# Performance work log

Hardware: AMD Instinct MI355X
Metric: run time of the kernel (lower is better)

Reference implementation:

```python
import jax, jax.numpy as jnp
import numpy as np

N_NODES = 10000
N_EDGES = 100000
IN_CH = 384
PROJ = 768  # in_channels * projection_factor
N_BLOCKS = 4
OUT_CH = 128
LN_EPS = 1e-5


def _p(key, shape, fan_in):
    return jax.random.normal(key, shape, dtype=jnp.float32) * (1.0 / np.sqrt(fan_in))


def setup_inputs() -> dict:
    key = jax.random.key(0)
    ks = iter(jax.random.split(key, 64))
    x = jax.random.normal(next(ks), (N_NODES, IN_CH), dtype=jnp.float32)
    edge_index = jax.random.randint(next(ks), (2, N_EDGES), 0, N_NODES, dtype=jnp.int64)
    inp = {
        'x': x,
        'edge_index': edge_index,
        'proj_W': _p(next(ks), (PROJ, IN_CH), IN_CH),
        'proj_b': jnp.zeros((PROJ,), jnp.float32),
        'norm_w': jnp.ones((N_BLOCKS, PROJ), jnp.float32),
        'norm_b': jnp.zeros((N_BLOCKS, PROJ), jnp.float32),
        'g1_W': _p(next(ks), (N_BLOCKS, 4 * 192, PROJ), PROJ),
        'g1_as': _p(next(ks), (N_BLOCKS, 4, 192), 192),
        'g1_ad': _p(next(ks), (N_BLOCKS, 4, 192), 192),
        'g1_b': jnp.zeros((N_BLOCKS, 4 * 192), jnp.float32),
        'g2_W': _p(next(ks), (N_BLOCKS, 2 * 96, PROJ), PROJ),
        'g2_as': _p(next(ks), (N_BLOCKS, 2, 96), 96),
        'g2_ad': _p(next(ks), (N_BLOCKS, 2, 96), 96),
        'g2_b': jnp.zeros((N_BLOCKS, 2 * 96), jnp.float32),
        'uni_W': _p(next(ks), (N_BLOCKS, PROJ, 960), 960),
        'uni_b': jnp.zeros((N_BLOCKS, PROJ), jnp.float32),
        'fnorm_w': jnp.ones((PROJ,), jnp.float32),
        'fnorm_b': jnp.zeros((PROJ,), jnp.float32),
        'fg_W': _p(next(ks), (8 * OUT_CH, PROJ), PROJ),
        'fg_as': _p(next(ks), (8, OUT_CH), OUT_CH),
        'fg_ad': _p(next(ks), (8, OUT_CH), OUT_CH),
        'fg_b': jnp.zeros((OUT_CH,), jnp.float32),
    }
    return inp


def layer_norm(x, w, b):
    m = x.mean(-1, keepdims=True)
    v = ((x - m) ** 2).mean(-1, keepdims=True)
    return (x - m) / jnp.sqrt(v + LN_EPS) * w + b


def gat_conv(x, src, dst, W, a_src, a_dst, bias, heads, out_ch, concat):
    # PyG GATConv (eval mode, add_self_loops already applied in src/dst).
    n = x.shape[0]
    h = (x @ W.T).reshape(n, heads, out_ch)          # [N,H,C]
    al_s = jnp.einsum('nhc,hc->nh', h, a_src)        # [N,H]
    al_d = jnp.einsum('nhc,hc->nh', h, a_dst)
    e = jax.nn.leaky_relu(al_s[src] + al_d[dst], 0.2)  # [E,H]
    emax = jax.ops.segment_max(e, dst, num_segments=n)
    ee = jnp.exp(e - emax[dst])
    den = jax.ops.segment_sum(ee, dst, num_segments=n)
    alpha = ee / (den[dst] + 1e-16)                  # softmax over incoming edges
    out = jax.ops.segment_sum(h[src] * alpha[:, :, None], dst, num_segments=n)
    out = out.reshape(n, heads * out_ch) if concat else out.mean(axis=1)
    return out + bias


def reference(x, edge_index, proj_W, proj_b, norm_w, norm_b,
              g1_W, g1_as, g1_ad, g1_b, g2_W, g2_as, g2_ad, g2_b,
              uni_W, uni_b, fnorm_w, fnorm_b, fg_W, fg_as, fg_ad, fg_b):
    n = x.shape[0]
    loop = jnp.arange(n, dtype=edge_index.dtype)
    src = jnp.concatenate([edge_index[0], loop])  # add self loops (PyG default)
    dst = jnp.concatenate([edge_index[1], loop])

    h = jax.nn.elu(x @ proj_W.T + proj_b)
    for i in range(N_BLOCKS):
        res = h
        hn = layer_norm(h, norm_w[i], norm_b[i])
        o1 = gat_conv(hn, src, dst, g1_W[i], g1_as[i], g1_ad[i], g1_b[i], 4, 192, True)
        o2 = gat_conv(hn, src, dst, g2_W[i], g2_as[i], g2_ad[i], g2_b[i], 2, 96, True)
        cat = jax.nn.elu(jnp.concatenate([o1, o2], axis=-1))  # [N,960]
        h = jax.nn.elu(res + cat @ uni_W[i].T + uni_b[i])
    h = layer_norm(h, fnorm_w, fnorm_b)
    return gat_conv(h, src, dst, fg_W, fg_as, fg_ad, fg_b, 8, OUT_CH, False)
```

## Files before the change

kernel.cpp:

```cpp
#include <hip/hip_runtime.h>
#include <math.h>

#define N_NODES 10000
#define N_EDGES 100000
#define E_TOT   (N_EDGES + N_NODES)
#define PROJ    768
#define LN_EPS  1e-5f

typedef __attribute__((ext_vector_type(8))) short bf16x8;
typedef __attribute__((ext_vector_type(4))) short bf16x4;
typedef __attribute__((ext_vector_type(4))) float f32x4;

__device__ __forceinline__ float elu_f(float x){ return x > 0.f ? x : __expf(x) - 1.f; }
__device__ __forceinline__ float bf2f(unsigned short u){ return __uint_as_float(((unsigned int)u) << 16); }
__device__ __forceinline__ unsigned short f2bf(float f){
  unsigned int u = __float_as_uint(f);
  return (unsigned short)((u + 0x7FFFu + ((u >> 16) & 1u)) >> 16);
}

#define GLOAD16(gp, lp) __builtin_amdgcn_global_load_lds((const __attribute__((address_space(1))) void*)(gp), (__attribute__((address_space(3))) void*)(lp), 16, 0, 0)

__global__ void k_count(const int* __restrict__ ei, int* __restrict__ cnt){
  int e = blockIdx.x*blockDim.x + threadIdx.x;
  if (e >= E_TOT) return;
  int dst = (e < N_EDGES) ? ei[N_EDGES + e] : (e - N_EDGES);
  atomicAdd(&cnt[dst], 1);
}

__global__ void k_scan(const int* __restrict__ cnt, int* __restrict__ indptr){
  __shared__ int s[1024];
  __shared__ int s_running;
  int t = threadIdx.x;
  if (t == 0) s_running = 0;
  __syncthreads();
  for (int base = 0; base < N_NODES; base += 1024){
    int v = (base + t < N_NODES) ? cnt[base + t] : 0;
    s[t] = v; __syncthreads();
    for (int off = 1; off < 1024; off <<= 1){
      int add = (t >= off) ? s[t - off] : 0;
      __syncthreads();
      s[t] += add;
      __syncthreads();
    }
    int total = s[1023];
    int run = s_running;
    if (base + t < N_NODES) indptr[base + t] = run + s[t] - v;
    __syncthreads();
    if (t == 0) s_running = run + total;
    __syncthreads();
  }
  if (t == 0) indptr[N_NODES] = s_running;
}

__global__ void k_copy_int(const int* __restrict__ src, int* __restrict__ dst, int n){
  int i = blockIdx.x*blockDim.x + threadIdx.x;
  if (i < n) dst[i] = src[i];
}

__global__ void k_fill(const int* __restrict__ ei, int* __restrict__ pos, int* __restrict__ csr_src){
  int e = blockIdx.x*blockDim.x + threadIdx.x;
  if (e >= E_TOT) return;
  int s, d;
  if (e < N_EDGES){ s = ei[e]; d = ei[N_EDGES + e]; }
  else            { s = d = e - N_EDGES; }
  int p = atomicAdd(&pos[d], 1);
  csr_src[p] = s;
}

__global__ void k_f2bf_arr4(const float4* __restrict__ in, ushort4* __restrict__ out, int n4){
  int i = blockIdx.x*blockDim.x + threadIdx.x;
  if (i < n4){
    float4 v = in[i];
    ushort4 o;
    o.x = f2bf(v.x); o.y = f2bf(v.y); o.z = f2bf(v.z); o.w = f2bf(v.w);
    out[i] = o;
  }
}

__global__ void k_pack_l1l2(const float* __restrict__ g1, const float* __restrict__ g2,
                            unsigned short* __restrict__ dst){
  int i = blockIdx.x*blockDim.x + threadIdx.x;
  if (i >= 737280) return;
  int layer = i / 184320;
  int off4  = i - layer*184320;
  float4 v;
  if (off4 < 147456) v = *((const float4*)(g1 + (size_t)layer*589824) + off4);
  else               v = *((const float4*)(g2 + (size_t)layer*147456) + (off4 - 147456));
  ushort4 o;
  o.x = f2bf(v.x); o.y = f2bf(v.y); o.z = f2bf(v.z); o.w = f2bf(v.w);
  ((ushort4*)(dst + (size_t)layer*737280))[off4] = o;
}

__global__ void k_layernorm_bf(const float* __restrict__ x, const float* __restrict__ w,
                               const float* __restrict__ b, unsigned short* __restrict__ y){
  int n = blockIdx.x;
  int t = threadIdx.x;
  const float* xr = x + (size_t)n*PROJ;
  float v0 = xr[t], v1 = xr[t+256], v2 = xr[t+512];
  float s  = v0+v1+v2;
  float s2 = v0*v0 + v1*v1 + v2*v2;
  #pragma unroll
  for (int off = 32; off; off >>= 1){ s += __shfl_down(s, off); s2 += __shfl_down(s2, off); }
  __shared__ float rs[4], rs2[4];
  __shared__ float s_mean, s_rstd;
  int wid = t >> 6, lane = t & 63;
  if (lane == 0){ rs[wid] = s; rs2[wid] = s2; }
  __syncthreads();
  if (t == 0){
    float S  = rs[0]+rs[1]+rs[2]+rs[3];
    float S2 = rs2[0]+rs2[1]+rs2[2]+rs2[3];
    float m  = S * (1.f/768.f);
    float var = S2 * (1.f/768.f) - m*m;
    s_mean = m; s_rstd = rsqrtf(var + LN_EPS);
  }
  __syncthreads();
  float m = s_mean, r = s_rstd;
  unsigned short* yr = y + (size_t)n*PROJ;
  yr[t]     = f2bf((v0-m)*r*w[t]     + b[t]);
  yr[t+256] = f2bf((v1-m)*r*w[t+256] + b[t+256]);
  yr[t+512] = f2bf((v2-m)*r*w[t+512] + b[t+512]);
}

template<int EPI>
__global__ __launch_bounds__(256, 2)
void k_gemm_mfma(const unsigned short* __restrict__ A, int lda,
                 const unsigned short* __restrict__ W,
                 void* __restrict__ Cv, int ldc,
                 int M, int N, int K,
                 const float* __restrict__ bias,
                 const float* __restrict__ res, int ldres, int NBN){
  __shared__ unsigned short As[2][128*64];
  __shared__ unsigned short Bs[2][128*64];
  const int tid = threadIdx.x;
  const int lane = tid & 63, wid = tid >> 6;
  const int wm = wid >> 1, wn = wid & 1;

  const int nwg = gridDim.x;
  const int q = nwg >> 3, r = nwg & 7;
  const int xcd = blockIdx.x & 7, o = blockIdx.x >> 3;
  const int swz = (xcd < r ? xcd*(q+1) : r*(q+1) + (xcd - r)*q) + o;
  const int bm = (swz / NBN) * 128;
  const int bn = (swz % NBN) * 128;

  const int srow = tid >> 3;
  const int sc16 = (tid & 7) ^ (srow & 7);
  size_t ga[4], gb[4];
  #pragma unroll
  for (int p = 0; p < 4; p++){
    ga[p] = (size_t)min(bm + p*32 + srow, M-1)*lda + sc16*8;
    gb[p] = (size_t)min(bn + p*32 + srow, N-1)*K   + sc16*8;
  }
  const int ldst = tid*8;

  f32x4 acc[4][4];
  #pragma unroll
  for (int i=0;i<4;i++)
    #pragma unroll
    for (int j=0;j<4;j++) acc[i][j] = (f32x4){0.f,0.f,0.f,0.f};

  const int rA = wm*64 + (lane & 15);
  const int rB = wn*64 + (lane & 15);

  const int NT = K >> 6;
  int cur = 0;
  #pragma unroll
  for (int p = 0; p < 4; p++){
    GLOAD16(A + ga[p], &As[0][p*2048 + ldst]);
    GLOAD16(W + gb[p], &Bs[0][p*2048 + ldst]);
  }
  for (int t = 0; t < NT; ++t){
    __syncthreads();
    if (t + 1 < NT){
      const int k0 = (t+1) << 6;
      #pragma unroll
      for (int p = 0; p < 4; p++){
        GLOAD16(A + ga[p] + k0, &As[cur^1][p*2048 + ldst]);
        GLOAD16(W + gb[p] + k0, &Bs[cur^1][p*2048 + ldst]);
      }
    }
    #pragma unroll
    for (int kk = 0; kk < 2; kk++){
      bf16x8 af[4], bfr[4];
      const int cA = (((kk<<2) | (lane>>4)) ^ (lane&7)) * 8;
      #pragma unroll
      for (int mi = 0; mi < 4; mi++)
        af[mi] = *(const bf16x8*)&As[cur][(rA + mi*16)*64 + cA];
      #pragma unroll
      for (int ni = 0; ni < 4; ni++)
        bfr[ni] = *(const bf16x8*)&Bs[cur][(rB + ni*16)*64 + cA];
      #pragma unroll
      for (int mi = 0; mi < 4; mi++)
        #pragma unroll
        for (int ni = 0; ni < 4; ni++)
          acc[mi][ni] = __builtin_amdgcn_mfma_f32_16x16x32_bf16(af[mi], bfr[ni], acc[mi][ni], 0,0,0);
    }
    cur ^= 1;
  }

  const int mrow0 = bm + wm*64 + ((lane>>4)<<2);
  const int ncol0 = bn + wn*64 + (lane & 15);
  #pragma unroll
  for (int mi=0; mi<4; mi++){
    #pragma unroll
    for (int rr=0; rr<4; rr++){
      int m = mrow0 + mi*16 + rr;
      if (m >= M) continue;
      #pragma unroll
      for (int ni=0; ni<4; ni++){
        int n = ncol0 + ni*16;
        if (n >= N) continue;
        float v = acc[mi][ni][rr];
        if (EPI == 0){
          ((unsigned short*)Cv)[(size_t)m*ldc + n] = f2bf(v);
        } else if (EPI == 1){
          ((float*)Cv)[(size_t)m*ldc + n] = elu_f(v + bias[n]);
        } else {
          ((float*)Cv)[(size_t)m*ldc + n] = elu_f(v + bias[n] + res[(size_t)m*ldres + n]);
        }
      }
    }
  }
}

template<int H, int C>
__global__ void k_attn_coef(const unsigned short* __restrict__ hlin, int ldh,
                            const float* __restrict__ a_src,
                            const float* __restrict__ a_dst,
                            float* __restrict__ als, float* __restrict__ ald){
  constexpr int CH = C/4;
  int n = blockIdx.x;
  int wid = threadIdx.x >> 6, lane = threadIdx.x & 63;
  float ss = 0.f, sd = 0.f;
  if (lane < CH){
    bf16x4 hv = *(const bf16x4*)(hlin + (size_t)n*ldh + wid*C + lane*4);
    float4 as_ = *(const float4*)&a_src[wid*C + lane*4];
    float4 ad_ = *(const float4*)&a_dst[wid*C + lane*4];
    float h0 = bf2f((unsigned short)hv.x), h1 = bf2f((unsigned short)hv.y);
    float h2 = bf2f((unsigned short)hv.z), h3 = bf2f((unsigned short)hv.w);
    ss = h0*as_.x + h1*as_.y + h2*as_.z + h3*as_.w;
    sd = h0*ad_.x + h1*ad_.y + h2*ad_.z + h3*ad_.w;
  }
  #pragma unroll
  for (int off = 32; off; off >>= 1){ ss += __shfl_down(ss, off); sd += __shfl_down(sd, off); }
  if (lane == 0){ als[n*H + wid] = ss; ald[n*H + wid] = sd; }
}

template<int H, int C, bool CONCAT, bool DO_ELU>
__global__ __launch_bounds__(256)
void k_attn_agg(const unsigned short* __restrict__ hlin, int ldh,
                const float* __restrict__ als, const float* __restrict__ ald,
                const int* __restrict__ indptr, const int* __restrict__ csr_src,
                const float* __restrict__ bias,
                void* __restrict__ outv, int ldo, int col0){
  constexpr int TOT = H*C;
  constexpr int CHUNKS = TOT/4;
  constexpr int CPL = (CHUNKS + 63)/64;
  int n = blockIdx.x;
  int tid = threadIdx.x;
  int wv = tid >> 6, lane = tid & 63;
  int beg = indptr[n], end = indptr[n+1];

  __shared__ float s_m[H], s_dinv[H], s_ald[H];
  __shared__ float s_red[4][TOT];

  for (int h = wv; h < H; h += 4){
    float aldv = ald[n*H + h];
    float m = -1e30f, d = 0.f;
    for (int e = beg + lane; e < end; e += 64){
      int s = csr_src[e];
      float v = als[s*H + h] + aldv;
      v = v > 0.f ? v : 0.2f*v;
      if (v > m){ d *= __expf(m - v); m = v; }
      d += __expf(v - m);
    }
    #pragma unroll
    for (int off = 1; off < 64; off <<= 1){
      float mo = __shfl_xor(m, off);
      float dd = __shfl_xor(d, off);
      float mn = fmaxf(m, mo);
      d = d*__expf(m - mn) + dd*__expf(mo - mn);
      m = mn;
    }
    if (lane == 0){ s_m[h] = m; s_dinv[h] = 1.f/(d + 1e-16f); s_ald[h] = aldv; }
  }
  __syncthreads();

  int hof[CPL];
  #pragma unroll
  for (int p = 0; p < CPL; p++) hof[p] = ((lane + p*64)*4)/C;

  f32x4 acc[CPL];
  #pragma unroll
  for (int p = 0; p < CPL; p++) acc[p] = (f32x4){0.f,0.f,0.f,0.f};

  for (int e = beg + wv; e < end; e += 4){
    int s = csr_src[e];
    float al = 0.f;
    if (lane < H){
      float v = als[s*H + lane] + s_ald[lane];
      v = v > 0.f ? v : 0.2f*v;
      al = __expf(v - s_m[lane]) * s_dinv[lane];
    }
    float aph[CPL];
    #pragma unroll
    for (int p = 0; p < CPL; p++) aph[p] = __shfl(al, hof[p]);
    const bf16x4* hr = (const bf16x4*)(hlin + (size_t)s*ldh);
    #pragma unroll
    for (int p = 0; p < CPL; p++){
      int ch = lane + p*64;
      if (CHUNKS % 64 == 0 || ch < CHUNKS){
        bf16x4 hv = hr[ch];
        acc[p].x += bf2f((unsigned short)hv.x)*aph[p];
        acc[p].y += bf2f((unsigned short)hv.y)*aph[p];
        acc[p].z += bf2f((unsigned short)hv.z)*aph[p];
        acc[p].w += bf2f((unsigned short)hv.w)*aph[p];
      }
    }
  }

  #pragma unroll
  for (int p = 0; p < CPL; p++){
    int ch = lane + p*64;
    if (CHUNKS % 64 == 0 || ch < CHUNKS)
      *(f32x4*)&s_red[wv][ch*4] = acc[p];
  }
  __syncthreads();

  if (CONCAT){
    unsigned short* out = (unsigned short*)outv;
    constexpr int QS = (TOT + 255)/256;
    #pragma unroll
    for (int qq = 0; qq < QS; qq++){
      int idx = tid + qq*256;
      if (TOT % 256 == 0 || idx < TOT){
        float v = s_red[0][idx] + s_red[1][idx] + s_red[2][idx] + s_red[3][idx] + bias[idx];
        if (DO_ELU) v = elu_f(v);
        out[(size_t)n*ldo + col0 + idx] = f2bf(v);
      }
    }
  } else {
    float* out = (float*)outv;
    if (tid < C){
      float v = 0.f;
      #pragma unroll
      for (int h = 0; h < H; h++){
        int idx = h*C + tid;
        v += s_red[0][idx] + s_red[1][idx] + s_red[2][idx] + s_red[3][idx];
      }
      out[(size_t)n*ldo + tid] = v*(1.f/(float)H) + bias[tid];
    }
  }
}

extern "C" void kernel_launch(void* const* d_in, const int* in_sizes, int n_in,
                              void* d_out, int out_size, void* d_ws, size_t ws_size,
                              hipStream_t stream){
  const float* x      = (const float*)d_in[0];
  const int*   ei     = (const int*)  d_in[1];
  const float* proj_W = (const float*)d_in[2];
  const float* proj_b = (const float*)d_in[3];
  const float* norm_w = (const float*)d_in[4];
  const float* norm_b = (const float*)d_in[5];
  const float* g1_W   = (const float*)d_in[6];
  const float* g1_as  = (const float*)d_in[7];
  const float* g1_ad  = (const float*)d_in[8];
  const float* g1_b   = (const float*)d_in[9];
  const float* g2_W   = (const float*)d_in[10];
  const float* g2_as  = (const float*)d_in[11];
  const float* g2_ad  = (const float*)d_in[12];
  const float* g2_b   = (const float*)d_in[13];
  const float* uni_W  = (const float*)d_in[14];
  const float* uni_b  = (const float*)d_in[15];
  const float* fnorm_w= (const float*)d_in[16];
  const float* fnorm_b= (const float*)d_in[17];
  const float* fg_W   = (const float*)d_in[18];
  const float* fg_as  = (const float*)d_in[19];
  const float* fg_ad  = (const float*)d_in[20];
  const float* fg_b   = (const float*)d_in[21];

  float* w = (float*)d_ws;
  float* h    = w; w += 7680000;
  float* h2   = w; w += 7680000;
  unsigned short* linbuf = (unsigned short*)w; w += 5120000;
  unsigned short* hnb  = (unsigned short*)w; w += 3840000;
  unsigned short* catb = (unsigned short*)w; w += 4800000;
  unsigned short* wb   = (unsigned short*)w; w += 3489792;
  float* als  = w; w += 80000;
  float* ald  = w; w += 80000;
  float* als2 = w; w += 80000;
  float* ald2 = w; w += 80000;
  int* iw = (int*)w;
  int* cnt     = iw; iw += 10016;
  int* indptr  = iw; iw += 10016;
  int* pos     = iw; iw += 10016;
  int* csr_src = iw; iw += 110016;

  unsigned short* wb_proj = wb;
  unsigned short* wb_l12  = wb_proj + 294912;
  unsigned short* wb_uni  = wb_l12 + 2949120;
  unsigned short* wb_fg   = wb_uni + 2949120;

  hipMemsetAsync(cnt, 0, N_NODES*sizeof(int), stream);
  k_count<<<(E_TOT+255)/256, 256, 0, stream>>>(ei, cnt);
  k_scan<<<1, 1024, 0, stream>>>(cnt, indptr);
  k_copy_int<<<(N_NODES+255)/256, 256, 0, stream>>>(indptr, pos, N_NODES);
  k_fill<<<(E_TOT+255)/256, 256, 0, stream>>>(ei, pos, csr_src);

  k_f2bf_arr4<<<(960000+255)/256, 256, 0, stream>>>((const float4*)x, (ushort4*)hnb, 960000);
  k_f2bf_arr4<<<(73728+255)/256,  256, 0, stream>>>((const float4*)proj_W, (ushort4*)wb_proj, 73728);
  k_pack_l1l2<<<(737280+255)/256, 256, 0, stream>>>(g1_W, g2_W, wb_l12);
  k_f2bf_arr4<<<(737280+255)/256, 256, 0, stream>>>((const float4*)uni_W, (ushort4*)wb_uni, 737280);
  k_f2bf_arr4<<<(196608+255)/256, 256, 0, stream>>>((const float4*)fg_W, (ushort4*)wb_fg, 196608);

  dim3 blk(256);
  const int GM = (N_NODES + 127) / 128;

  k_gemm_mfma<1><<<dim3(6*GM), blk, 0, stream>>>(hnb, 384, wb_proj, h, 768, N_NODES, 768, 384, proj_b, nullptr, 0, 6);

  float* cur = h;
  float* oth = h2;
  for (int i = 0; i < 4; i++){
    k_layernorm_bf<<<N_NODES, 256, 0, stream>>>(cur, norm_w + i*768, norm_b + i*768, hnb);
    k_gemm_mfma<0><<<dim3(8*GM), blk, 0, stream>>>(hnb, 768, wb_l12 + (size_t)i*737280, linbuf, 960, N_NODES, 960, 768, nullptr, nullptr, 0, 8);
    k_attn_coef<4,192><<<N_NODES, 256, 0, stream>>>(linbuf, 960, g1_as + i*768, g1_ad + i*768, als, ald);
    k_attn_agg<4,192,true,true><<<N_NODES, 256, 0, stream>>>(linbuf, 960, als, ald, indptr, csr_src, g1_b + i*768, catb, 960, 0);
    k_attn_coef<2,96><<<N_NODES, 128, 0, stream>>>(linbuf + 768, 960, g2_as + i*192, g2_ad + i*192, als2, ald2);
    k_attn_agg<2,96,true,true><<<N_NODES, 256, 0, stream>>>(linbuf + 768, 960, als2, ald2, indptr, csr_src, g2_b + i*192, catb, 960, 768);
    k_gemm_mfma<2><<<dim3(6*GM), blk, 0, stream>>>(catb, 960, wb_uni + (size_t)i*737280, oth, 768, N_NODES, 768, 960, uni_b + i*768, cur, 768, 6);
    float* t = cur; cur = oth; oth = t;
  }

  k_layernorm_bf<<<N_NODES, 256, 0, stream>>>(cur, fnorm_w, fnorm_b, hnb);
  k_gemm_mfma<0><<<dim3(8*GM), blk, 0, stream>>>(hnb, 768, wb_fg, linbuf, 1024, N_NODES, 1024, 768, nullptr, nullptr, 0, 8);
  k_attn_coef<8,128><<<N_NODES, 512, 0, stream>>>(linbuf, 1024, fg_as, fg_ad, als, ald);
  k_attn_agg<8,128,false,false><<<N_NODES, 256, 0, stream>>>(linbuf, 1024, als, ald, indptr, csr_src, fg_b, d_out, 128, 0);
}
```

Baseline: 789.6 us.

## Merge both GAT convs into one aggregation pass with precomputed edge alphas

Fuses the two per-block GAT aggregations (4x192 and 2x96 heads) into a single kernel over 960 columns, so each edge's source row is gathered once per block instead of twice. Softmax statistics move to a separate per-node kernel, and a per-edge kernel materialises normalized alpha values using a new csr_dst array. The aggregation loop then reads alpha from memory instead of recomputing exp and shuffling per edge. In exchange it adds two extra launches per block and an alpha buffer write and read, and the aggregation no longer runs the first softmax pass inline.

Result: no change. 803.5 us (+1.8%).

```diff
diff --git a/kernel.cpp b/kernel.cpp
--- a/kernel.cpp
+++ b/kernel.cpp
@@ -57,7 +57,8 @@
   if (i < n) dst[i] = src[i];
 }
 
-__global__ void k_fill(const int* __restrict__ ei, int* __restrict__ pos, int* __restrict__ csr_src){
+__global__ void k_fill(const int* __restrict__ ei, int* __restrict__ pos,
+                       int* __restrict__ csr_src, int* __restrict__ csr_dst){
   int e = blockIdx.x*blockDim.x + threadIdx.x;
   if (e >= E_TOT) return;
   int s, d;
@@ -65,6 +66,7 @@
   else            { s = d = e - N_EDGES; }
   int p = atomicAdd(&pos[d], 1);
   csr_src[p] = s;
+  csr_dst[p] = d;
 }
 
 __global__ void k_f2bf_arr4(const float4* __restrict__ in, ushort4* __restrict__ out, int n4){
@@ -222,7 +224,7 @@
   }
 }
 
-template<int H, int C>
+template<int H, int C, int ST, int OFF>
 __global__ void k_attn_coef(const unsigned short* __restrict__ hlin, int ldh,
                             const float* __restrict__ a_src,
                             const float* __restrict__ a_dst,
@@ -242,17 +244,59 @@
   }
   #pragma unroll
   for (int off = 32; off; off >>= 1){ ss += __shfl_down(ss, off); sd += __shfl_down(sd, off); }
-  if (lane == 0){ als[n*H + wid] = ss; ald[n*H + wid] = sd; }
-}
-
-template<int H, int C, bool CONCAT, bool DO_ELU>
+  if (lane == 0){ als[n*ST + OFF + wid] = ss; ald[n*ST + OFF + wid] = sd; }
+}
+
+template<int HT>
+__global__ void k_attn_stats(const float* __restrict__ als, const float* __restrict__ ald,
+                             const int* __restrict__ indptr, const int* __restrict__ csr_src,
+                             float* __restrict__ mo, float* __restrict__ dio){
+  int n = blockIdx.x;
+  int wv = threadIdx.x >> 6, lane = threadIdx.x & 63;
+  int beg = indptr[n], end = indptr[n+1];
+  float aldv = ald[n*HT + wv];
+  float m = -1e30f, d = 0.f;
+  for (int e = beg + lane; e < end; e += 64){
+    int s = csr_src[e];
+    float v = als[s*HT + wv] + aldv;
+    v = v > 0.f ? v : 0.2f*v;
+    if (v > m){ d *= __expf(m - v); m = v; }
+    d += __expf(v - m);
+  }
+  #pragma unroll
+  for (int off = 1; off < 64; off <<= 1){
+    float mo_ = __shfl_xor(m, off);
+    float dd  = __shfl_xor(d, off);
+    float mn  = fmaxf(m, mo_);
+    d = d*__expf(m - mn) + dd*__expf(mo_ - mn);
+    m = mn;
+  }
+  if (lane == 0){ mo[n*HT + wv] = m; dio[n*HT + wv] = 1.f/(d + 1e-16f); }
+}
+
+template<int HT>
+__global__ void k_attn_alpha(const float* __restrict__ als, const float* __restrict__ ald,
+                             const int* __restrict__ csr_src, const int* __restrict__ csr_dst,
+                             const float* __restrict__ m, const float* __restrict__ dinv,
+                             float* __restrict__ alpha){
+  int i = blockIdx.x*blockDim.x + threadIdx.x;
+  if (i >= E_TOT*HT) return;
+  int e = i / HT, h = i - e*HT;
+  int s = csr_src[e], d = csr_dst[e];
+  float v = als[s*HT + h] + ald[d*HT + h];
+  v = v > 0.f ? v : 0.2f*v;
+  alpha[i] = __expf(v - m[d*HT + h]) * dinv[d*HT + h];
+}
+
+template<int MODE>
 __global__ __launch_bounds__(256)
-void k_attn_agg(const unsigned short* __restrict__ hlin, int ldh,
-                const float* __restrict__ als, const float* __restrict__ ald,
-                const int* __restrict__ indptr, const int* __restrict__ csr_src,
-                const float* __restrict__ bias,
-                void* __restrict__ outv, int ldo, int col0){
-  constexpr int TOT = H*C;
+void k_attn_agg2(const unsigned short* __restrict__ hlin, int ldh,
+                 const float* __restrict__ alpha,
+                 const int* __restrict__ indptr, const int* __restrict__ csr_src,
+                 const float* __restrict__ b1, const float* __restrict__ b2,
+                 void* __restrict__ outv, int ldo){
+  constexpr int TOT = MODE ? 1024 : 960;
+  constexpr int HT  = MODE ? 8 : 6;
   constexpr int CHUNKS = TOT/4;
   constexpr int CPL = (CHUNKS + 63)/64;
   int n = blockIdx.x;
@@ -260,34 +304,14 @@
   int wv = tid >> 6, lane = tid & 63;
   int beg = indptr[n], end = indptr[n+1];
 
-  __shared__ float s_m[H], s_dinv[H], s_ald[H];
   __shared__ float s_red[4][TOT];
 
-  for (int h = wv; h < H; h += 4){
-    float aldv = ald[n*H + h];
-    float m = -1e30f, d = 0.f;
-    for (int e = beg + lane; e < end; e += 64){
-      int s = csr_src[e];
-      float v = als[s*H + h] + aldv;
-      v = v > 0.f ? v : 0.2f*v;
-      if (v > m){ d *= __expf(m - v); m = v; }
-      d += __expf(v - m);
-    }
-    #pragma unroll
-    for (int off = 1; off < 64; off <<= 1){
-      float mo = __shfl_xor(m, off);
-      float dd = __shfl_xor(d, off);
-      float mn = fmaxf(m, mo);
-      d = d*__expf(m - mn) + dd*__expf(mo - mn);
-      m = mn;
-    }
-    if (lane == 0){ s_m[h] = m; s_dinv[h] = 1.f/(d + 1e-16f); s_ald[h] = aldv; }
-  }
-  __syncthreads();
-
   int hof[CPL];
   #pragma unroll
-  for (int p = 0; p < CPL; p++) hof[p] = ((lane + p*64)*4)/C;
+  for (int p = 0; p < CPL; p++){
+    int ch4 = (lane + p*64)*4;
+    hof[p] = MODE ? (ch4 >> 7) : (ch4 < 768 ? ch4/192 : 4 + (ch4-768)/96);
+  }
 
   f32x4 acc[CPL];
   #pragma unroll
@@ -295,25 +319,18 @@
 
   for (int e = beg + wv; e < end; e += 4){
     int s = csr_src[e];
-    float al = 0.f;
-    if (lane < H){
-      float v = als[s*H + lane] + s_ald[lane];
-      v = v > 0.f ? v : 0.2f*v;
-      al = __expf(v - s_m[lane]) * s_dinv[lane];
-    }
-    float aph[CPL];
-    #pragma unroll
-    for (int p = 0; p < CPL; p++) aph[p] = __shfl(al, hof[p]);
     const bf16x4* hr = (const bf16x4*)(hlin + (size_t)s*ldh);
+    const float* ae = alpha + (size_t)e*HT;
     #pragma unroll
     for (int p = 0; p < CPL; p++){
       int ch = lane + p*64;
       if (CHUNKS % 64 == 0 || ch < CHUNKS){
+        float al = ae[hof[p]];
         bf16x4 hv = hr[ch];
-        acc[p].x += bf2f((unsigned short)hv.x)*aph[p];
-        acc[p].y += bf2f((unsigned short)hv.y)*aph[p];
-        acc[p].z += bf2f((unsigned short)hv.z)*aph[p];
-        acc[p].w += bf2f((unsigned short)hv.w)*aph[p];
+        acc[p].x += bf2f((unsigned short)hv.x)*al;
+        acc[p].y += bf2f((unsigned short)hv.y)*al;
+        acc[p].z += bf2f((unsigned short)hv.z)*al;
+        acc[p].w += bf2f((unsigned short)hv.w)*al;
       }
     }
   }
@@ -326,28 +343,27 @@
   }
   __syncthreads();
 
-  if (CONCAT){
+  if (MODE == 0){
     unsigned short* out = (unsigned short*)outv;
-    constexpr int QS = (TOT + 255)/256;
     #pragma unroll
-    for (int qq = 0; qq < QS; qq++){
+    for (int qq = 0; qq < 4; qq++){
       int idx = tid + qq*256;
-      if (TOT % 256 == 0 || idx < TOT){
-        float v = s_red[0][idx] + s_red[1][idx] + s_red[2][idx] + s_red[3][idx] + bias[idx];
-        if (DO_ELU) v = elu_f(v);
-        out[(size_t)n*ldo + col0 + idx] = f2bf(v);
+      if (idx < TOT){
+        float bb = idx < 768 ? b1[idx] : b2[idx - 768];
+        float v = s_red[0][idx] + s_red[1][idx] + s_red[2][idx] + s_red[3][idx] + bb;
+        out[(size_t)n*ldo + idx] = f2bf(elu_f(v));
       }
     }
   } else {
     float* out = (float*)outv;
-    if (tid < C){
+    if (tid < 128){
       float v = 0.f;
       #pragma unroll
-      for (int h = 0; h < H; h++){
-        int idx = h*C + tid;
+      for (int h = 0; h < 8; h++){
+        int idx = h*128 + tid;
         v += s_red[0][idx] + s_red[1][idx] + s_red[2][idx] + s_red[3][idx];
       }
-      out[(size_t)n*ldo + tid] = v*(1.f/(float)H) + bias[tid];
+      out[(size_t)n*ldo + tid] = v*0.125f + b1[tid];
     }
   }
 }
@@ -385,15 +401,17 @@
   unsigned short* hnb  = (unsigned short*)w; w += 3840000;
   unsigned short* catb = (unsigned short*)w; w += 4800000;
   unsigned short* wb   = (unsigned short*)w; w += 3489792;
-  float* als  = w; w += 80000;
-  float* ald  = w; w += 80000;
-  float* als2 = w; w += 80000;
-  float* ald2 = w; w += 80000;
+  float* als   = w; w += 80000;
+  float* ald   = w; w += 80000;
+  float* mbuf  = w; w += 80000;
+  float* dibuf = w; w += 80000;
+  float* alphab= w; w += 880000;
   int* iw = (int*)w;
   int* cnt     = iw; iw += 10016;
   int* indptr  = iw; iw += 10016;
   int* pos     = iw; iw += 10016;
   int* csr_src = iw; iw += 110016;
+  int* csr_dst = iw; iw += 110016;
 
   unsigned short* wb_proj = wb;
   unsigned short* wb_l12  = wb_proj + 294912;
@@ -404,7 +422,7 @@
   k_count<<<(E_TOT+255)/256, 256, 0, stream>>>(ei, cnt);
   k_scan<<<1, 1024, 0, stream>>>(cnt, indptr);
   k_copy_int<<<(N_NODES+255)/256, 256, 0, stream>>>(indptr, pos, N_NODES);
-  k_fill<<<(E_TOT+255)/256, 256, 0, stream>>>(ei, pos, csr_src);
+  k_fill<<<(E_TOT+255)/256, 256, 0, stream>>>(ei, pos, csr_src, csr_dst);
 
   k_f2bf_arr4<<<(960000+255)/256, 256, 0, stream>>>((const float4*)x, (ushort4*)hnb, 960000);
   k_f2bf_arr4<<<(73728+255)/256,  256, 0, stream>>>((const float4*)proj_W, (ushort4*)wb_proj, 73728);
@@ -422,16 +440,19 @@
   for (int i = 0; i < 4; i++){
     k_layernorm_bf<<<N_NODES, 256, 0, stream>>>(cur, norm_w + i*768, norm_b + i*768, hnb);
     k_gemm_mfma<0><<<dim3(8*GM), blk, 0, stream>>>(hnb, 768, wb_l12 + (size_t)i*737280, linbuf, 960, N_NODES, 960, 768, nullptr, nullptr, 0, 8);
-    k_attn_coef<4,192><<<N_NODES, 256, 0, stream>>>(linbuf, 960, g1_as + i*768, g1_ad + i*768, als, ald);
-    k_attn_agg<4,192,true,true><<<N_NODES, 256, 0, stream>>>(linbuf, 960, als, ald, indptr, csr_src, g1_b + i*768, catb, 960, 0);
-    k_attn_coef<2,96><<<N_NODES, 128, 0, stream>>>(linbuf + 768, 960, g2_as + i*192, g2_ad + i*192, als2, ald2);
-    k_attn_agg<2,96,true,true><<<N_NODES, 256, 0, stream>>>(linbuf + 768, 960, als2, ald2, indptr, csr_src, g2_b + i*192, catb, 960, 768);
+    k_attn_coef<4,192,6,0><<<N_NODES, 256, 0, stream>>>(linbuf, 960, g1_as + i*768, g1_ad + i*768, als, ald);
+    k_attn_coef<2,96,6,4><<<N_NODES, 128, 0, stream>>>(linbuf + 768, 960, g2_as + i*192, g2_ad + i*192, als, ald);
+    k_attn_stats<6><<<N_NODES, 384, 0, stream>>>(als, ald, indptr, csr_src, mbuf, dibuf);
+    k_attn_alpha<6><<<(E_TOT*6+255)/256, 256, 0, stream>>>(als, ald, csr_src, csr_dst, mbuf, dibuf, alphab);
+    k_attn_agg2<0><<<N_NODES, 256, 0, stream>>>(linbuf, 960, alphab, indptr, csr_src, g1_b + i*768, g2_b + i*192, catb, 960);
     k_gemm_mfma<2><<<dim3(6*GM), blk, 0, stream>>>(catb, 960, wb_uni + (size_t)i*737280, oth, 768, N_NODES, 768, 960, uni_b + i*768, cur, 768, 6);
     float* t = cur; cur = oth; oth = t;
   }
 
   k_layernorm_bf<<<N_NODES, 256, 0, stream>>>(cur, fnorm_w, fnorm_b, hnb);
   k_gemm_mfma<0><<<dim3(8*GM), blk, 0, stream>>>(hnb, 768, wb_fg, linbuf, 1024, N_NODES, 1024, 768, nullptr, nullptr, 0, 8);
-  k_attn_coef<8,128><<<N_NODES, 512, 0, stream>>>(linbuf, 1024, fg_as, fg_ad, als, ald);
-  k_attn_agg<8,128,false,false><<<N_NODES, 256, 0, stream>>>(linbuf, 1024, als, ald, indptr, csr_src, fg_b, d_out, 128, 0);
-}
+  k_attn_coef<8,128,8,0><<<N_NODES, 512, 0, stream>>>(linbuf, 1024, fg_as, fg_ad, als, ald);
+  k_attn_stats<8><<<N_NODES, 512, 0, stream>>>(als, ald, indptr, csr_src, mbuf, dibuf);
+  k_attn_alpha<8><<<(E_TOT*8+255)/256, 256, 0, stream>>>(als, ald, csr_src, csr_dst, mbuf, dibuf, alphab);
+  k_attn_agg2<1><<<N_NODES, 256, 0, stream>>>(linbuf, 1024, alphab, indptr, csr_src, fg_b, nullptr, d_out, 128);
+}
```
